# Performance work log

Hardware: AMD Instinct MI355X
Metric: run time of the kernel (lower is better)

## Reference

```python
import jax, jax.numpy as jnp
import numpy as np

N_EVENTS = 16384   # original pixel events
D = 128            # input_size
H = 128            # hidden_size
K = 9              # kernel 3x3 -> patch coords
S = 2048           # number of patch sequences
LMAX = 108         # max sequence length
T = 147456         # total patch events = sum(lengths) = 9 * N_EVENTS


def setup_inputs() -> dict:
    key = jax.random.key(0)
    ks = jax.random.split(key, 8)
    events = jax.random.normal(ks[0], (N_EVENTS, D), jnp.float32)
    pos_id = jax.random.randint(ks[1], (T,), 0, K, dtype=jnp.int32)
    orig_event_idx = jax.random.randint(ks[2], (T,), 0, N_EVENTS, dtype=jnp.int32)
    # alternating 36/108 lengths: 1024*36 + 1024*108 = 147456 = T
    lengths = jnp.where(jnp.arange(S) % 2 == 0, 36, 108).astype(jnp.int32)
    std = float(np.sqrt(2.0 / (D + H)))
    scatter_w = jax.random.normal(ks[3], (K, H, D), jnp.float32) * std
    gather_w = jax.random.normal(ks[4], (K, H, H), jnp.float32) * std
    lstm_std = float(1.0 / np.sqrt(H))
    w_ih = jax.random.uniform(ks[5], (4 * H, H), jnp.float32, -lstm_std, lstm_std)
    w_hh = jax.random.uniform(ks[6], (4 * H, H), jnp.float32, -lstm_std, lstm_std)
    ln_g = jnp.ones((H,), jnp.float32)
    ln_b = jnp.zeros((H,), jnp.float32)
    return dict(events=events, scatter_w=scatter_w, gather_w=gather_w,
                w_ih=w_ih, w_hh=w_hh, ln_g=ln_g, ln_b=ln_b,
                pos_id=pos_id, orig_event_idx=orig_event_idx, lengths=lengths)


def _pos_proj(x, W, pos_id):
    # position-indexed projection: out[t] = W[pos_id[t]] @ x[t]
    # loop over small fixed K=9 with masked accumulate (matches the torch loop)
    out = jnp.zeros((x.shape[0], W.shape[1]), x.dtype)
    for k in range(W.shape[0]):
        out = out + jnp.where((pos_id == k)[:, None], x @ W[k].T, 0.0)
    return out


def reference(events, scatter_w, gather_w, w_ih, w_hh, ln_g, ln_b,
              pos_id, orig_event_idx, lengths):
    # scatter events to patch replicas
    x = events[orig_event_idx]                           # [T, D]
    x = _pos_proj(x, scatter_w, pos_id)                  # [T, H]

    # flat (sequence-major) -> padded [S, LMAX, H]
    seq_offsets = jnp.cumsum(lengths) - lengths          # [S]
    seq_ids = jnp.repeat(jnp.arange(S), lengths, total_repeat_length=T)
    pos_in_seq = jnp.arange(T) - seq_offsets[seq_ids]
    padded = jnp.zeros((S, LMAX, H), x.dtype).at[seq_ids, pos_in_seq].set(x)

    # single-layer bias-free LSTM (pytorch gate order i, f, g, o), zero init.
    # zero-padding after each sequence's valid region leaves valid outputs
    # identical to a PackedSequence LSTM.
    def step(carry, xt):                                 # xt: [S, H]
        h, c = carry
        gates = xt @ w_ih.T + h @ w_hh.T                 # [S, 4H]
        i, f, g, o = jnp.split(gates, 4, axis=-1)
        c = jax.nn.sigmoid(f) * c + jax.nn.sigmoid(i) * jnp.tanh(g)
        h = jax.nn.sigmoid(o) * jnp.tanh(c)
        return (h, c), h

    init = (jnp.zeros((S, H), x.dtype), jnp.zeros((S, H), x.dtype))
    _, hs = jax.lax.scan(step, init, jnp.swapaxes(padded, 0, 1))  # [LMAX, S, H]
    o_flat = jnp.swapaxes(hs, 0, 1)[seq_ids, pos_in_seq]          # [T, H]

    o_flat = _pos_proj(o_flat, gather_w, pos_id)                  # [T, H]

    # gather patch events back to pixel events (scatter-add) + residual + LN
    out = jnp.zeros((N_EVENTS, H), x.dtype).at[orig_event_idx].add(o_flat)
    out = out + events                                   # input_proj is None (D == H)
    mu = jnp.mean(out, axis=-1, keepdims=True)
    var = jnp.var(out, axis=-1, keepdims=True)
    out = (out - mu) * jax.lax.rsqrt(var + 1e-5) * ln_g + ln_b
    return out
```

## Files before the change

kernel.cpp:

```cpp
#include <hip/hip_runtime.h>

#define N_EVENTS 16384
#define DIM 128
#define NK 9
#define NSEQ 2048
#define TT 147456
#define CHUNK 64
#define NCHUNK_MAX (TT/CHUNK + NK)
#define NHBLK 576

typedef __attribute__((ext_vector_type(8))) short bf16x8;
typedef __attribute__((ext_vector_type(4))) float f32x4;
typedef __attribute__((ext_vector_type(4))) int i32x4;

#define OFF_EV     0UL
#define OFF_WC     (OFF_EV   + (size_t)N_EVENTS*DIM*2)
#define OFF_SCAT   (OFF_WC   + (size_t)512*256*2)
#define OFF_GATH   (OFF_SCAT + (size_t)NK*DIM*DIM*2)
#define OFF_XS     (OFF_GATH + (size_t)NK*DIM*DIM*2)
#define OFF_HS     (OFF_XS   + (size_t)TT*DIM*2)
#define OFF_KLIST  (OFF_HS   + (size_t)TT*DIM*2)
#define OFF_ACC    (OFF_KLIST+ (size_t)TT*4)
#define OFF_SEQOFF (OFF_ACC  + (size_t)N_EVENTS*DIM*4)
#define OFF_GROUP  (OFF_SEQOFF + (size_t)NSEQ*4)
#define OFF_MISC   (OFF_GROUP  + (size_t)NSEQ*4)
#define OFF_BH     (OFF_MISC   + 256UL)

__device__ __forceinline__ short f2b(float f) {
    union { float f; unsigned u; } v; v.f = f;
    unsigned r = (v.u + 0x7FFFu + ((v.u >> 16) & 1u)) >> 16;
    return (short)r;
}

__device__ __forceinline__ float fsig(float x) {
    return __builtin_amdgcn_rcpf(1.f + __expf(-x));
}
__device__ __forceinline__ float ftanh(float x) {
    return 1.f - 2.f * __builtin_amdgcn_rcpf(__expf(2.f * x) + 1.f);
}

__global__ void convert_kernel(const float* __restrict__ ev, const float* __restrict__ wih,
                               const float* __restrict__ whh, const float* __restrict__ sw,
                               const float* __restrict__ gw,
                               short* __restrict__ evb, short* __restrict__ wcb,
                               short* __restrict__ swb, short* __restrict__ gwb,
                               float* __restrict__ acc) {
    int idx = blockIdx.x * blockDim.x + threadIdx.x;
    if (idx < N_EVENTS * DIM) { evb[idx] = f2b(ev[idx]); acc[idx] = 0.f; }
    if (idx < 512 * DIM) {
        int j = idx >> 7, d = idx & 127;
        wcb[j * 256 + d]       = f2b(wih[idx]);
        wcb[j * 256 + 128 + d] = f2b(whh[idx]);
    }
    if (idx < NK * DIM * DIM) { swb[idx] = f2b(sw[idx]); gwb[idx] = f2b(gw[idx]); }
}

__global__ void hist_kernel(const int* __restrict__ pos, int* __restrict__ blockhist) {
    __shared__ int h[NK];
    int tid = threadIdx.x;
    if (tid < NK) h[tid] = 0;
    __syncthreads();
    atomicAdd(&h[pos[blockIdx.x * 256 + tid]], 1);
    __syncthreads();
    if (tid < NK) blockhist[blockIdx.x * NK + tid] = h[tid];
}

__global__ void scan_kernel(int* __restrict__ blockhist, int* __restrict__ misc) {
    __shared__ int h[NHBLK * NK];
    int tid = threadIdx.x;
    for (int i = tid; i < NHBLK * NK; i += 256) h[i] = blockhist[i];
    __syncthreads();
    if (tid < NK) {
        int run = 0;
        for (int b = 0; b < NHBLK; b++) {
            int v = h[b * NK + tid];
            h[b * NK + tid] = run;
            run += v;
        }
        misc[tid] = run;
    }
    __syncthreads();
    if (tid == 0) {
        int ko = 0, co = 0;
        for (int k = 0; k < NK; k++) {
            int c = misc[k];
            misc[32 + k] = ko;
            misc[48 + k] = co;
            ko += c;
            co += (c + CHUNK - 1) / CHUNK;
        }
        misc[48 + NK] = co;
    }
    __syncthreads();
    for (int i = tid; i < NHBLK * NK; i += 256) blockhist[i] = h[i];
}

__global__ void setup_kernel(const int* __restrict__ lengths,
                             int* __restrict__ seq_off, int* __restrict__ grouped) {
    __shared__ int lens[NSEQ];
    __shared__ int tsum[256], tlong[256];
    int tid = threadIdx.x;
    for (int i = tid; i < NSEQ; i += 256) lens[i] = lengths[i];
    __syncthreads();
    int base = tid * 8;
    int ls[8]; int s = 0, lc = 0;
    #pragma unroll
    for (int i = 0; i < 8; i++) { ls[i] = lens[base + i]; s += ls[i]; lc += (ls[i] > 64) ? 1 : 0; }
    tsum[tid] = s; tlong[tid] = lc;
    __syncthreads();
    for (int d = 1; d < 256; d <<= 1) {
        int a = (tid >= d) ? tsum[tid - d] : 0;
        int b = (tid >= d) ? tlong[tid - d] : 0;
        __syncthreads();
        tsum[tid] += a; tlong[tid] += b;
        __syncthreads();
    }
    int nlong_total = tlong[255];
    int excl = tsum[tid] - s;
    int excl_long = tlong[tid] - lc;
    int run = 0, runl = 0;
    #pragma unroll
    for (int i = 0; i < 8; i++) {
        int sid = base + i;
        seq_off[sid] = excl + run;
        int longs_before = excl_long + runl;
        if (ls[i] > 64) { grouped[longs_before] = sid; runl++; }
        else            { grouped[nlong_total + (sid - longs_before)] = sid; }
        run += ls[i];
    }
}

__global__ void fill2_kernel(const int* __restrict__ pos, const int* __restrict__ blockhist,
                             const int* __restrict__ misc, int* __restrict__ klist) {
    __shared__ int off[NK];
    int tid = threadIdx.x;
    if (tid < NK) off[tid] = misc[32 + tid] + blockhist[blockIdx.x * NK + tid];
    __syncthreads();
    int t = blockIdx.x * 256 + tid;
    int p = atomicAdd(&off[pos[t]], 1);
    klist[p] = t;
}

__global__ void bucket_gemm(const short* __restrict__ src, const short* __restrict__ wall,
                            const int* __restrict__ klist, const int* __restrict__ misc,
                            const int* __restrict__ orig, short* __restrict__ xs_out,
                            float* __restrict__ acc, int mode) {
    const int* chunkoff = misc + 48;
    int b = blockIdx.x;
    if (b >= chunkoff[NK]) return;
    int k = 0;
    while (k < NK - 1 && chunkoff[k + 1] <= b) k++;
    int lc = b - chunkoff[k];
    int cnt = misc[k];
    int base = misc[32 + k] + lc * CHUNK;
    int nv = min(CHUNK, cnt - lc * CHUNK);

    __shared__ int tok[CHUNK], dst[CHUNK];
    __shared__ short A[CHUNK * 136];
    int tid = threadIdx.x;
    if (tid < CHUNK) {
        int tv = klist[base + ((tid < nv) ? tid : 0)];
        tok[tid] = tv;
        dst[tid] = orig[tv];
    }
    __syncthreads();
    {
        int row = tid >> 2, part = tid & 3;
        int ridx = (mode == 0) ? dst[row] : tok[row];
        const i32x4* s4 = (const i32x4*)(src + (size_t)ridx * DIM + part * 32);
        i32x4* d4 = (i32x4*)(A + row * 136 + part * 32);
        d4[0] = s4[0]; d4[1] = s4[1]; d4[2] = s4[2]; d4[3] = s4[3];
    }
    __syncthreads();
    int wave = tid >> 6, lane = tid & 63, l15 = lane & 15, q = lane >> 4;
    const short* wk = wall + (size_t)k * DIM * DIM;
    bf16x8 Bf[2][4];
    #pragma unroll
    for (int nt = 0; nt < 2; nt++) {
        int h = wave * 32 + nt * 16 + l15;
        #pragma unroll
        for (int kt = 0; kt < 4; kt++)
            Bf[nt][kt] = *(const bf16x8*)(wk + h * DIM + kt * 32 + q * 8);
    }
    f32x4 C[4][2];
    #pragma unroll
    for (int mt = 0; mt < 4; mt++)
        #pragma unroll
        for (int nt = 0; nt < 2; nt++) C[mt][nt] = (f32x4){0.f, 0.f, 0.f, 0.f};
    #pragma unroll
    for (int mt = 0; mt < 4; mt++) {
        bf16x8 Afr[4];
        const short* ar = A + (mt * 16 + l15) * 136 + q * 8;
        Afr[0] = *(const bf16x8*)(ar);
        Afr[1] = *(const bf16x8*)(ar + 32);
        Afr[2] = *(const bf16x8*)(ar + 64);
        Afr[3] = *(const bf16x8*)(ar + 96);
        #pragma unroll
        for (int nt = 0; nt < 2; nt++)
            #pragma unroll
            for (int kt = 0; kt < 4; kt++)
                C[mt][nt] = __builtin_amdgcn_mfma_f32_16x16x32_bf16(Afr[kt], Bf[nt][kt], C[mt][nt], 0, 0, 0);
    }
    if (mode == 0) {
        __syncthreads();
        #pragma unroll
        for (int mt = 0; mt < 4; mt++)
            #pragma unroll
            for (int nt = 0; nt < 2; nt++)
                #pragma unroll
                for (int r = 0; r < 4; r++) {
                    int row = mt * 16 + q * 4 + r;
                    int col = wave * 32 + nt * 16 + l15;
                    A[row * 136 + col] = f2b(C[mt][nt][r]);
                }
        __syncthreads();
        int row = tid >> 2, part = tid & 3;
        if (row < nv) {
            const i32x4* s4 = (const i32x4*)(A + row * 136 + part * 32);
            i32x4* d4 = (i32x4*)(xs_out + (size_t)tok[row] * DIM + part * 32);
            d4[0] = s4[0]; d4[1] = s4[1]; d4[2] = s4[2]; d4[3] = s4[3];
        }
    } else {
        #pragma unroll
        for (int mt = 0; mt < 4; mt++)
            #pragma unroll
            for (int nt = 0; nt < 2; nt++)
                #pragma unroll
                for (int r = 0; r < 4; r++) {
                    int row = mt * 16 + q * 4 + r;
                    if (row < nv) {
                        int col = wave * 32 + nt * 16 + l15;
                        atomicAdd(acc + (size_t)dst[row] * DIM + col, C[mt][nt][r]);
                    }
                }
    }
}

#define MF(a, b, c) __builtin_amdgcn_mfma_f32_16x16x32_bf16(a, b, c, 0, 0, 0)

#define LSTM_STEP(J, PF) { \
    const int i_ = ib8 + (J); \
    f32x4 Cxi = {0.f,0.f,0.f,0.f}, Cxf = {0.f,0.f,0.f,0.f}; \
    f32x4 Cxg = {0.f,0.f,0.f,0.f}, Cxo = {0.f,0.f,0.f,0.f}; \
    Cxi = MF(PF[0], Bf[0][0], Cxi); Cxf = MF(PF[0], Bf[1][0], Cxf); \
    Cxg = MF(PF[0], Bf[2][0], Cxg); Cxo = MF(PF[0], Bf[3][0], Cxo); \
    Cxi = MF(PF[1], Bf[0][1], Cxi); Cxf = MF(PF[1], Bf[1][1], Cxf); \
    Cxg = MF(PF[1], Bf[2][1], Cxg); Cxo = MF(PF[1], Bf[3][1], Cxo); \
    Cxi = MF(PF[2], Bf[0][2], Cxi); Cxf = MF(PF[2], Bf[1][2], Cxf); \
    Cxg = MF(PF[2], Bf[2][2], Cxg); Cxo = MF(PF[2], Bf[3][2], Cxo); \
    Cxi = MF(PF[3], Bf[0][3], Cxi); Cxf = MF(PF[3], Bf[1][3], Cxf); \
    Cxg = MF(PF[3], Bf[2][3], Cxg); Cxo = MF(PF[3], Bf[3][3], Cxo); \
    bf16x8 Hf0, Hf1, Hf2, Hf3; \
    { const short* hp_ = hb + (((J) + 7) & 7) * 1088 + l15 * 136 + ql * 8; \
      Hf0 = *(const bf16x8*)(hp_);      Hf1 = *(const bf16x8*)(hp_ + 32); \
      Hf2 = *(const bf16x8*)(hp_ + 64); Hf3 = *(const bf16x8*)(hp_ + 96); } \
    f32x4 Chi = {0.f,0.f,0.f,0.f}, Chf = {0.f,0.f,0.f,0.f}; \
    f32x4 Chg = {0.f,0.f,0.f,0.f}, Cho = {0.f,0.f,0.f,0.f}; \
    Chi = MF(Hf0, Bf[0][4], Chi); Chf = MF(Hf0, Bf[1][4], Chf); \
    Chg = MF(Hf0, Bf[2][4], Chg); Cho = MF(Hf0, Bf[3][4], Cho); \
    Chi = MF(Hf1, Bf[0][5], Chi); Chf = MF(Hf1, Bf[1][5], Chf); \
    Chg = MF(Hf1, Bf[2][5], Chg); Cho = MF(Hf1, Bf[3][5], Cho); \
    Chi = MF(Hf2, Bf[0][6], Chi); Chf = MF(Hf2, Bf[1][6], Chf); \
    Chg = MF(Hf2, Bf[2][6], Chg); Cho = MF(Hf2, Bf[3][6], Cho); \
    Chi = MF(Hf3, Bf[0][7], Chi); Chf = MF(Hf3, Bf[1][7], Chf); \
    Chg = MF(Hf3, Bf[2][7], Chg); Cho = MF(Hf3, Bf[3][7], Cho); \
    if (l15 < 8) { \
        const short* xp_ = xs + xoff; \
        PF[0] = *(const bf16x8*)(xp_);      PF[1] = *(const bf16x8*)(xp_ + 32); \
        PF[2] = *(const bf16x8*)(xp_ + 64); PF[3] = *(const bf16x8*)(xp_ + 96); \
    } \
    xoff += ((i_ + 4) <= my_len) ? DIM : 0; \
    f32x4 Gi = Cxi + Chi, Gf = Cxf + Chf, Gg = Cxg + Chg, Go = Cxo + Cho; \
    { \
        int src_ = lane & 31; \
        float i2 = __shfl(Gi[2], src_, 64), i3 = __shfl(Gi[3], src_, 64); \
        float f2 = __shfl(Gf[2], src_, 64), f3 = __shfl(Gf[3], src_, 64); \
        float g2 = __shfl(Gg[2], src_, 64), g3 = __shfl(Gg[3], src_, 64); \
        float o2 = __shfl(Go[2], src_, 64), o3 = __shfl(Go[3], src_, 64); \
        float iA = lo ? Gi[0] : i2, iB = lo ? Gi[1] : i3; \
        float fA = lo ? Gf[0] : f2, fB = lo ? Gf[1] : f3; \
        float gA = lo ? Gg[0] : g2, gB = lo ? Gg[1] : g3; \
        float oA = lo ? Go[0] : o2, oB = lo ? Go[1] : o3; \
        if (i_ < lenA) { \
            float si = fsig(iA), sf = fsig(fA), so = fsig(oA); \
            float tg = ftanh(gA); \
            float cn = sf * cA + si * tg; \
            float th = ftanh(cn); \
            cA = cn; \
            hb[(J) * 1088 + rowA * 136 + u] = f2b(so * th); \
        } \
        if (i_ < lenB) { \
            float si = fsig(iB), sf = fsig(fB), so = fsig(oB); \
            float tg = ftanh(gB); \
            float cn = sf * cB + si * tg; \
            float th = ftanh(cn); \
            cB = cn; \
            hb[(J) * 1088 + rowB * 136 + u] = f2b(so * th); \
        } \
    } \
    __syncthreads(); \
}

__global__ __launch_bounds__(512, 2) void lstm_kernel(
        const short* __restrict__ xs, const short* __restrict__ wc,
        short* __restrict__ hstore, const int* __restrict__ seq_off,
        const int* __restrict__ grouped, const int* __restrict__ lengths) {
    __shared__ int s_off[8], s_len[8];
    __shared__ short hchunk[11][8][136];
    int tid = threadIdx.x;
    if (tid < 8) {
        int s = grouped[blockIdx.x * 8 + tid];
        s_off[tid] = seq_off[s];
        s_len[tid] = lengths[s];
    }
    for (int j = tid; j < 11 * 8 * 136; j += 512) ((short*)hchunk)[j] = 0;
    __syncthreads();
    int lane = tid & 63, l15 = lane & 15, ql = lane >> 4;
    int wave = tid >> 6;
    int u = wave * 16 + l15;
    short* hb = (short*)hchunk;
    bf16x8 Bf[4][8];
    #pragma unroll
    for (int g = 0; g < 4; g++) {
        int j = g * 128 + u;
        #pragma unroll
        for (int kt = 0; kt < 8; kt++)
            Bf[g][kt] = *(const bf16x8*)(wc + j * 256 + kt * 32 + ql * 8);
    }
    int maxlen = 0;
    #pragma unroll
    for (int i = 0; i < 8; i++) maxlen = max(maxlen, s_len[i]);
    int my_off = (l15 < 8) ? s_off[l15] : 0;
    int my_len = (l15 < 8) ? s_len[l15] : 1;
    bool lo = (ql < 2);
    int rowA = lo ? (ql * 4 + 0) : ((ql - 2) * 4 + 2);
    int rowB = lo ? (ql * 4 + 1) : ((ql - 2) * 4 + 3);
    int lenA = s_len[rowA], lenB = s_len[rowB];
    float cA = 0.f, cB = 0.f;
    bf16x8 Pf0[4], Pf1[4];
    #pragma unroll
    for (int k = 0; k < 4; k++) { Pf0[k] = (bf16x8){0,0,0,0,0,0,0,0}; Pf1[k] = Pf0[k]; }
    int xoff = my_off * DIM + ql * 8;
    if (l15 < 8) {
        const short* xp = xs + xoff;
        Pf0[0] = *(const bf16x8*)(xp);      Pf0[1] = *(const bf16x8*)(xp + 32);
        Pf0[2] = *(const bf16x8*)(xp + 64); Pf0[3] = *(const bf16x8*)(xp + 96);
    }
    int xoff1 = xoff + ((my_len > 1) ? DIM : 0);
    if (l15 < 8) {
        const short* xp = xs + xoff1;
        Pf1[0] = *(const bf16x8*)(xp);      Pf1[1] = *(const bf16x8*)(xp + 32);
        Pf1[2] = *(const bf16x8*)(xp + 64); Pf1[3] = *(const bf16x8*)(xp + 96);
    }
    xoff = xoff1 + ((my_len > 2) ? DIM : 0);

    int nb8 = (maxlen + 7) >> 3;
    for (int ob = 0; ob < nb8; ob++) {
        int ib8 = ob * 8;
        LSTM_STEP(0, Pf0)
        LSTM_STEP(1, Pf1)
        LSTM_STEP(2, Pf0)
        LSTM_STEP(3, Pf1)
        LSTM_STEP(4, Pf0)
        LSTM_STEP(5, Pf1)
        LSTM_STEP(6, Pf0)
        LSTM_STEP(7, Pf1)
        #pragma unroll
        for (int it = 0; it < 2; it++) {
            int idx = tid + it * 512;
            int st = idx >> 7, s = (idx >> 4) & 7, part = idx & 15;
            int ig = ib8 + st;
            if (ig < s_len[s]) {
                i32x4 v = *(const i32x4*)&hchunk[st][s][part * 8];
                *(i32x4*)(hstore + (size_t)(s_off[s] + ig) * DIM + part * 8) = v;
            }
        }
        __syncthreads();
    }
}

__global__ void ln_kernel(const float* __restrict__ acc, const float* __restrict__ events,
                          const float* __restrict__ g, const float* __restrict__ bta,
                          float* __restrict__ out) {
    int tid = threadIdx.x;
    int wave = tid >> 6, lane = tid & 63;
    int e = blockIdx.x * 4 + wave;
    const float2* a2 = (const float2*)(acc + (size_t)e * DIM);
    const float2* e2 = (const float2*)(events + (size_t)e * DIM);
    float2 av = a2[lane], ev = e2[lane];
    float x0 = av.x + ev.x, x1 = av.y + ev.y;
    float sm = x0 + x1, sq = x0 * x0 + x1 * x1;
    #pragma unroll
    for (int m = 1; m < 64; m <<= 1) {
        sm += __shfl_xor(sm, m, 64);
        sq += __shfl_xor(sq, m, 64);
    }
    float mean = sm * (1.f / DIM);
    float var = sq * (1.f / DIM) - mean * mean;
    float rs = rsqrtf(var + 1e-5f);
    float2 gv = ((const float2*)g)[lane], bv = ((const float2*)bta)[lane];
    float2 ov;
    ov.x = (x0 - mean) * rs * gv.x + bv.x;
    ov.y = (x1 - mean) * rs * gv.y + bv.y;
    ((float2*)(out + (size_t)e * DIM))[lane] = ov;
}

extern "C" void kernel_launch(void* const* d_in, const int* in_sizes, int n_in,
                              void* d_out, int out_size, void* d_ws, size_t ws_size,
                              hipStream_t stream) {
    const float* events = (const float*)d_in[0];
    const float* scat   = (const float*)d_in[1];
    const float* gath   = (const float*)d_in[2];
    const float* wih    = (const float*)d_in[3];
    const float* whh    = (const float*)d_in[4];
    const float* lng    = (const float*)d_in[5];
    const float* lnb    = (const float*)d_in[6];
    const int* posid    = (const int*)d_in[7];
    const int* orig     = (const int*)d_in[8];
    const int* lens     = (const int*)d_in[9];
    char* ws = (char*)d_ws;
    short* evb   = (short*)(ws + OFF_EV);
    short* wcb   = (short*)(ws + OFF_WC);
    short* swb   = (short*)(ws + OFF_SCAT);
    short* gwb   = (short*)(ws + OFF_GATH);
    short* xs    = (short*)(ws + OFF_XS);
    short* hs    = (short*)(ws + OFF_HS);
    int*   klist = (int*)(ws + OFF_KLIST);
    float* acc   = (float*)(ws + OFF_ACC);
    int*   seqo  = (int*)(ws + OFF_SEQOFF);
    int*   grp   = (int*)(ws + OFF_GROUP);
    int*   misc  = (int*)(ws + OFF_MISC);
    int*   bh    = (int*)(ws + OFF_BH);
    float* out   = (float*)d_out;

    convert_kernel<<<8192, 256, 0, stream>>>(events, wih, whh, scat, gath, evb, wcb, swb, gwb, acc);
    hist_kernel<<<NHBLK, 256, 0, stream>>>(posid, bh);
    scan_kernel<<<1, 256, 0, stream>>>(bh, misc);
    setup_kernel<<<1, 256, 0, stream>>>(lens, seqo, grp);
    fill2_kernel<<<NHBLK, 256, 0, stream>>>(posid, bh, misc, klist);
    bucket_gemm<<<NCHUNK_MAX, 256, 0, stream>>>(evb, swb, klist, misc, orig, xs, nullptr, 0);
    lstm_kernel<<<256, 512, 0, stream>>>(xs, wcb, hs, seqo, grp, lens);
    bucket_gemm<<<NCHUNK_MAX, 256, 0, stream>>>(hs, gwb, klist, misc, orig, nullptr, acc, 1);
    ln_kernel<<<4096, 256, 0, stream>>>(acc, events, lng, lnb, out);
}
```

Before: 317.7 us.

## Fuse all pipeline stages into one cooperative persistent kernel with grid syncs

New measurement: 506.9 us. 1.6x slower.

```diff
diff --git a/kernel.cpp b/kernel.cpp
--- a/kernel.cpp
+++ b/kernel.cpp
@@ -1,4 +1,7 @@
 #include <hip/hip_runtime.h>
+#include <hip/hip_cooperative_groups.h>
+
+namespace cg = cooperative_groups;
 
 #define N_EVENTS 16384
 #define DIM 128
@@ -6,8 +9,9 @@
 #define NSEQ 2048
 #define TT 147456
 #define CHUNK 64
-#define NCHUNK_MAX (TT/CHUNK + NK)
-#define NHBLK 576
+#define NBLK 256
+#define TPB 512
+#define TOKB 576
 
 typedef __attribute__((ext_vector_type(8))) short bf16x8;
 typedef __attribute__((ext_vector_type(4))) float f32x4;
@@ -26,12 +30,19 @@
 #define OFF_MISC   (OFF_GROUP  + (size_t)NSEQ*4)
 #define OFF_BH     (OFF_MISC   + 256UL)
 
+struct MegaParams {
+    const float *ev, *sw, *gw, *wih, *whh, *lng, *lnb;
+    const int *pos, *orig, *lens;
+    short *evb, *wcb, *swb, *gwb, *xs, *hs;
+    int *klist, *misc, *bh, *seqo, *grp;
+    float *acc, *out;
+};
+
 __device__ __forceinline__ short f2b(float f) {
     union { float f; unsigned u; } v; v.f = f;
     unsigned r = (v.u + 0x7FFFu + ((v.u >> 16) & 1u)) >> 16;
     return (short)r;
 }
-
 __device__ __forceinline__ float fsig(float x) {
     return __builtin_amdgcn_rcpf(1.f + __expf(-x));
 }
@@ -39,125 +50,20 @@
     return 1.f - 2.f * __builtin_amdgcn_rcpf(__expf(2.f * x) + 1.f);
 }
 
-__global__ void convert_kernel(const float* __restrict__ ev, const float* __restrict__ wih,
-                               const float* __restrict__ whh, const float* __restrict__ sw,
-                               const float* __restrict__ gw,
-                               short* __restrict__ evb, short* __restrict__ wcb,
-                               short* __restrict__ swb, short* __restrict__ gwb,
-                               float* __restrict__ acc) {
-    int idx = blockIdx.x * blockDim.x + threadIdx.x;
-    if (idx < N_EVENTS * DIM) { evb[idx] = f2b(ev[idx]); acc[idx] = 0.f; }
-    if (idx < 512 * DIM) {
-        int j = idx >> 7, d = idx & 127;
-        wcb[j * 256 + d]       = f2b(wih[idx]);
-        wcb[j * 256 + 128 + d] = f2b(whh[idx]);
-    }
-    if (idx < NK * DIM * DIM) { swb[idx] = f2b(sw[idx]); gwb[idx] = f2b(gw[idx]); }
-}
-
-__global__ void hist_kernel(const int* __restrict__ pos, int* __restrict__ blockhist) {
-    __shared__ int h[NK];
-    int tid = threadIdx.x;
-    if (tid < NK) h[tid] = 0;
-    __syncthreads();
-    atomicAdd(&h[pos[blockIdx.x * 256 + tid]], 1);
-    __syncthreads();
-    if (tid < NK) blockhist[blockIdx.x * NK + tid] = h[tid];
-}
-
-__global__ void scan_kernel(int* __restrict__ blockhist, int* __restrict__ misc) {
-    __shared__ int h[NHBLK * NK];
-    int tid = threadIdx.x;
-    for (int i = tid; i < NHBLK * NK; i += 256) h[i] = blockhist[i];
-    __syncthreads();
-    if (tid < NK) {
-        int run = 0;
-        for (int b = 0; b < NHBLK; b++) {
-            int v = h[b * NK + tid];
-            h[b * NK + tid] = run;
-            run += v;
-        }
-        misc[tid] = run;
-    }
-    __syncthreads();
-    if (tid == 0) {
-        int ko = 0, co = 0;
-        for (int k = 0; k < NK; k++) {
-            int c = misc[k];
-            misc[32 + k] = ko;
-            misc[48 + k] = co;
-            ko += c;
-            co += (c + CHUNK - 1) / CHUNK;
-        }
-        misc[48 + NK] = co;
-    }
-    __syncthreads();
-    for (int i = tid; i < NHBLK * NK; i += 256) blockhist[i] = h[i];
-}
-
-__global__ void setup_kernel(const int* __restrict__ lengths,
-                             int* __restrict__ seq_off, int* __restrict__ grouped) {
-    __shared__ int lens[NSEQ];
-    __shared__ int tsum[256], tlong[256];
-    int tid = threadIdx.x;
-    for (int i = tid; i < NSEQ; i += 256) lens[i] = lengths[i];
-    __syncthreads();
-    int base = tid * 8;
-    int ls[8]; int s = 0, lc = 0;
+#define MF(a, b, c) __builtin_amdgcn_mfma_f32_16x16x32_bf16(a, b, c, 0, 0, 0)
+
+__device__ __forceinline__ void bucket_chunk(
+        int c, const int* choff, const short* src, const short* wall,
+        const int* klist, const int* misc, const int* orig,
+        short* xs_out, float* acc, int mode,
+        int* tok, int* dst, short* A, int tid) {
+    int k = 0;
     #pragma unroll
-    for (int i = 0; i < 8; i++) { ls[i] = lens[base + i]; s += ls[i]; lc += (ls[i] > 64) ? 1 : 0; }
-    tsum[tid] = s; tlong[tid] = lc;
-    __syncthreads();
-    for (int d = 1; d < 256; d <<= 1) {
-        int a = (tid >= d) ? tsum[tid - d] : 0;
-        int b = (tid >= d) ? tlong[tid - d] : 0;
-        __syncthreads();
-        tsum[tid] += a; tlong[tid] += b;
-        __syncthreads();
-    }
-    int nlong_total = tlong[255];
-    int excl = tsum[tid] - s;
-    int excl_long = tlong[tid] - lc;
-    int run = 0, runl = 0;
-    #pragma unroll
-    for (int i = 0; i < 8; i++) {
-        int sid = base + i;
-        seq_off[sid] = excl + run;
-        int longs_before = excl_long + runl;
-        if (ls[i] > 64) { grouped[longs_before] = sid; runl++; }
-        else            { grouped[nlong_total + (sid - longs_before)] = sid; }
-        run += ls[i];
-    }
-}
-
-__global__ void fill2_kernel(const int* __restrict__ pos, const int* __restrict__ blockhist,
-                             const int* __restrict__ misc, int* __restrict__ klist) {
-    __shared__ int off[NK];
-    int tid = threadIdx.x;
-    if (tid < NK) off[tid] = misc[32 + tid] + blockhist[blockIdx.x * NK + tid];
-    __syncthreads();
-    int t = blockIdx.x * 256 + tid;
-    int p = atomicAdd(&off[pos[t]], 1);
-    klist[p] = t;
-}
-
-__global__ void bucket_gemm(const short* __restrict__ src, const short* __restrict__ wall,
-                            const int* __restrict__ klist, const int* __restrict__ misc,
-                            const int* __restrict__ orig, short* __restrict__ xs_out,
-                            float* __restrict__ acc, int mode) {
-    const int* chunkoff = misc + 48;
-    int b = blockIdx.x;
-    if (b >= chunkoff[NK]) return;
-    int k = 0;
-    while (k < NK - 1 && chunkoff[k + 1] <= b) k++;
-    int lc = b - chunkoff[k];
+    for (int j = 1; j < NK; j++) k += (choff[j] <= c) ? 1 : 0;
+    int lc = c - choff[k];
     int cnt = misc[k];
     int base = misc[32 + k] + lc * CHUNK;
     int nv = min(CHUNK, cnt - lc * CHUNK);
-
-    __shared__ int tok[CHUNK], dst[CHUNK];
-    __shared__ short A[CHUNK * 136];
-    int tid = threadIdx.x;
     if (tid < CHUNK) {
         int tv = klist[base + ((tid < nv) ? tid : 0)];
         tok[tid] = tv;
@@ -165,78 +71,62 @@
     }
     __syncthreads();
     {
-        int row = tid >> 2, part = tid & 3;
+        int row = tid >> 3, part = tid & 7;
         int ridx = (mode == 0) ? dst[row] : tok[row];
-        const i32x4* s4 = (const i32x4*)(src + (size_t)ridx * DIM + part * 32);
-        i32x4* d4 = (i32x4*)(A + row * 136 + part * 32);
-        d4[0] = s4[0]; d4[1] = s4[1]; d4[2] = s4[2]; d4[3] = s4[3];
+        const i32x4* s4 = (const i32x4*)(src + (size_t)ridx * DIM + part * 16);
+        i32x4* d4 = (i32x4*)(A + row * 136 + part * 16);
+        d4[0] = s4[0]; d4[1] = s4[1];
     }
     __syncthreads();
-    int wave = tid >> 6, lane = tid & 63, l15 = lane & 15, q = lane >> 4;
+    int w = tid >> 6, lane = tid & 63, l15 = lane & 15, q = lane >> 4;
     const short* wk = wall + (size_t)k * DIM * DIM;
-    bf16x8 Bf[2][4];
+    int h = w * 16 + l15;
+    bf16x8 Bfr[4];
     #pragma unroll
-    for (int nt = 0; nt < 2; nt++) {
-        int h = wave * 32 + nt * 16 + l15;
-        #pragma unroll
-        for (int kt = 0; kt < 4; kt++)
-            Bf[nt][kt] = *(const bf16x8*)(wk + h * DIM + kt * 32 + q * 8);
-    }
-    f32x4 C[4][2];
+    for (int kt = 0; kt < 4; kt++)
+        Bfr[kt] = *(const bf16x8*)(wk + h * DIM + kt * 32 + q * 8);
+    f32x4 C[4];
     #pragma unroll
-    for (int mt = 0; mt < 4; mt++)
-        #pragma unroll
-        for (int nt = 0; nt < 2; nt++) C[mt][nt] = (f32x4){0.f, 0.f, 0.f, 0.f};
+    for (int mt = 0; mt < 4; mt++) C[mt] = (f32x4){0.f, 0.f, 0.f, 0.f};
     #pragma unroll
     for (int mt = 0; mt < 4; mt++) {
-        bf16x8 Afr[4];
         const short* ar = A + (mt * 16 + l15) * 136 + q * 8;
-        Afr[0] = *(const bf16x8*)(ar);
-        Afr[1] = *(const bf16x8*)(ar + 32);
-        Afr[2] = *(const bf16x8*)(ar + 64);
-        Afr[3] = *(const bf16x8*)(ar + 96);
-        #pragma unroll
-        for (int nt = 0; nt < 2; nt++)
-            #pragma unroll
-            for (int kt = 0; kt < 4; kt++)
-                C[mt][nt] = __builtin_amdgcn_mfma_f32_16x16x32_bf16(Afr[kt], Bf[nt][kt], C[mt][nt], 0, 0, 0);
+        bf16x8 A0 = *(const bf16x8*)(ar);
+        bf16x8 A1 = *(const bf16x8*)(ar + 32);
+        bf16x8 A2 = *(const bf16x8*)(ar + 64);
+        bf16x8 A3 = *(const bf16x8*)(ar + 96);
+        C[mt] = MF(A0, Bfr[0], C[mt]);
+        C[mt] = MF(A1, Bfr[1], C[mt]);
+        C[mt] = MF(A2, Bfr[2], C[mt]);
+        C[mt] = MF(A3, Bfr[3], C[mt]);
     }
     if (mode == 0) {
         __syncthreads();
         #pragma unroll
         for (int mt = 0; mt < 4; mt++)
             #pragma unroll
-            for (int nt = 0; nt < 2; nt++)
-                #pragma unroll
-                for (int r = 0; r < 4; r++) {
-                    int row = mt * 16 + q * 4 + r;
-                    int col = wave * 32 + nt * 16 + l15;
-                    A[row * 136 + col] = f2b(C[mt][nt][r]);
-                }
-        __syncthreads();
-        int row = tid >> 2, part = tid & 3;
+            for (int r = 0; r < 4; r++)
+                A[(mt * 16 + q * 4 + r) * 136 + h] = f2b(C[mt][r]);
+        __syncthreads();
+        int row = tid >> 3, part = tid & 7;
         if (row < nv) {
-            const i32x4* s4 = (const i32x4*)(A + row * 136 + part * 32);
-            i32x4* d4 = (i32x4*)(xs_out + (size_t)tok[row] * DIM + part * 32);
-            d4[0] = s4[0]; d4[1] = s4[1]; d4[2] = s4[2]; d4[3] = s4[3];
-        }
+            const i32x4* s4 = (const i32x4*)(A + row * 136 + part * 16);
+            i32x4* d4 = (i32x4*)(xs_out + (size_t)tok[row] * DIM + part * 16);
+            d4[0] = s4[0]; d4[1] = s4[1];
+        }
+        __syncthreads();
     } else {
         #pragma unroll
         for (int mt = 0; mt < 4; mt++)
             #pragma unroll
-            for (int nt = 0; nt < 2; nt++)
-                #pragma unroll
-                for (int r = 0; r < 4; r++) {
-                    int row = mt * 16 + q * 4 + r;
-                    if (row < nv) {
-                        int col = wave * 32 + nt * 16 + l15;
-                        atomicAdd(acc + (size_t)dst[row] * DIM + col, C[mt][nt][r]);
-                    }
-                }
-    }
-}
-
-#define MF(a, b, c) __builtin_amdgcn_mfma_f32_16x16x32_bf16(a, b, c, 0, 0, 0)
+            for (int r = 0; r < 4; r++) {
+                int row = mt * 16 + q * 4 + r;
+                if (row < nv)
+                    atomicAdd(acc + (size_t)dst[row] * DIM + h, C[mt][r]);
+            }
+        __syncthreads();
+    }
+}
 
 #define LSTM_STEP(J, PF) { \
     const int i_ = ib8 + (J); \
@@ -265,7 +155,7 @@
     Chi = MF(Hf3, Bf[0][7], Chi); Chf = MF(Hf3, Bf[1][7], Chf); \
     Chg = MF(Hf3, Bf[2][7], Chg); Cho = MF(Hf3, Bf[3][7], Cho); \
     if (l15 < 8) { \
-        const short* xp_ = xs + xoff; \
+        const short* xp_ = xsl + xoff; \
         PF[0] = *(const bf16x8*)(xp_);      PF[1] = *(const bf16x8*)(xp_ + 32); \
         PF[2] = *(const bf16x8*)(xp_ + 64); PF[3] = *(const bf16x8*)(xp_ + 96); \
     } \
@@ -301,145 +191,281 @@
     __syncthreads(); \
 }
 
-__global__ __launch_bounds__(512, 2) void lstm_kernel(
-        const short* __restrict__ xs, const short* __restrict__ wc,
-        short* __restrict__ hstore, const int* __restrict__ seq_off,
-        const int* __restrict__ grouped, const int* __restrict__ lengths) {
+__global__ __launch_bounds__(TPB, 2) void mega_kernel(MegaParams p) {
+    cg::grid_group grid = cg::this_grid();
+    __shared__ int hist9[NK];
+    __shared__ int hsc[NBLK * NK];
+    __shared__ int cnt9[NK];
+    __shared__ int lensS[NSEQ];
+    __shared__ int tsum[256], tlong[256];
+    __shared__ int offb[NK];
+    __shared__ int tok[CHUNK], dst[CHUNK];
+    __shared__ short Atile[CHUNK * 136];
+    __shared__ short hchunk[11 * 8 * 136];
     __shared__ int s_off[8], s_len[8];
-    __shared__ short hchunk[11][8][136];
-    int tid = threadIdx.x;
-    if (tid < 8) {
-        int s = grouped[blockIdx.x * 8 + tid];
-        s_off[tid] = seq_off[s];
-        s_len[tid] = lengths[s];
-    }
-    for (int j = tid; j < 11 * 8 * 136; j += 512) ((short*)hchunk)[j] = 0;
+
+    const int bid = blockIdx.x, tid = threadIdx.x;
+    const int gtid = bid * TPB + tid;
+
+    for (int i = gtid; i < N_EVENTS * DIM; i += NBLK * TPB) {
+        p.evb[i] = f2b(p.ev[i]);
+        p.acc[i] = 0.f;
+    }
+    if (gtid < 512 * DIM) {
+        int j = gtid >> 7, d = gtid & 127;
+        p.wcb[j * 256 + d]       = f2b(p.wih[gtid]);
+        p.wcb[j * 256 + 128 + d] = f2b(p.whh[gtid]);
+    }
+    for (int i = gtid; i < NK * DIM * DIM; i += NBLK * TPB) {
+        p.swb[i] = f2b(p.sw[i]);
+        p.gwb[i] = f2b(p.gw[i]);
+    }
+    if (tid < NK) hist9[tid] = 0;
     __syncthreads();
-    int lane = tid & 63, l15 = lane & 15, ql = lane >> 4;
-    int wave = tid >> 6;
-    int u = wave * 16 + l15;
-    short* hb = (short*)hchunk;
-    bf16x8 Bf[4][8];
-    #pragma unroll
-    for (int g = 0; g < 4; g++) {
-        int j = g * 128 + u;
-        #pragma unroll
-        for (int kt = 0; kt < 8; kt++)
-            Bf[g][kt] = *(const bf16x8*)(wc + j * 256 + kt * 32 + ql * 8);
-    }
-    int maxlen = 0;
-    #pragma unroll
-    for (int i = 0; i < 8; i++) maxlen = max(maxlen, s_len[i]);
-    int my_off = (l15 < 8) ? s_off[l15] : 0;
-    int my_len = (l15 < 8) ? s_len[l15] : 1;
-    bool lo = (ql < 2);
-    int rowA = lo ? (ql * 4 + 0) : ((ql - 2) * 4 + 2);
-    int rowB = lo ? (ql * 4 + 1) : ((ql - 2) * 4 + 3);
-    int lenA = s_len[rowA], lenB = s_len[rowB];
-    float cA = 0.f, cB = 0.f;
-    bf16x8 Pf0[4], Pf1[4];
-    #pragma unroll
-    for (int k = 0; k < 4; k++) { Pf0[k] = (bf16x8){0,0,0,0,0,0,0,0}; Pf1[k] = Pf0[k]; }
-    int xoff = my_off * DIM + ql * 8;
-    if (l15 < 8) {
-        const short* xp = xs + xoff;
-        Pf0[0] = *(const bf16x8*)(xp);      Pf0[1] = *(const bf16x8*)(xp + 32);
-        Pf0[2] = *(const bf16x8*)(xp + 64); Pf0[3] = *(const bf16x8*)(xp + 96);
-    }
-    int xoff1 = xoff + ((my_len > 1) ? DIM : 0);
-    if (l15 < 8) {
-        const short* xp = xs + xoff1;
-        Pf1[0] = *(const bf16x8*)(xp);      Pf1[1] = *(const bf16x8*)(xp + 32);
-        Pf1[2] = *(const bf16x8*)(xp + 64); Pf1[3] = *(const bf16x8*)(xp + 96);
-    }
-    xoff = xoff1 + ((my_len > 2) ? DIM : 0);
-
-    int nb8 = (maxlen + 7) >> 3;
-    for (int ob = 0; ob < nb8; ob++) {
-        int ib8 = ob * 8;
-        LSTM_STEP(0, Pf0)
-        LSTM_STEP(1, Pf1)
-        LSTM_STEP(2, Pf0)
-        LSTM_STEP(3, Pf1)
-        LSTM_STEP(4, Pf0)
-        LSTM_STEP(5, Pf1)
-        LSTM_STEP(6, Pf0)
-        LSTM_STEP(7, Pf1)
-        #pragma unroll
-        for (int it = 0; it < 2; it++) {
-            int idx = tid + it * 512;
-            int st = idx >> 7, s = (idx >> 4) & 7, part = idx & 15;
-            int ig = ib8 + st;
-            if (ig < s_len[s]) {
-                i32x4 v = *(const i32x4*)&hchunk[st][s][part * 8];
-                *(i32x4*)(hstore + (size_t)(s_off[s] + ig) * DIM + part * 8) = v;
-            }
-        }
-        __syncthreads();
-    }
-}
-
-__global__ void ln_kernel(const float* __restrict__ acc, const float* __restrict__ events,
-                          const float* __restrict__ g, const float* __restrict__ bta,
-                          float* __restrict__ out) {
-    int tid = threadIdx.x;
-    int wave = tid >> 6, lane = tid & 63;
-    int e = blockIdx.x * 4 + wave;
-    const float2* a2 = (const float2*)(acc + (size_t)e * DIM);
-    const float2* e2 = (const float2*)(events + (size_t)e * DIM);
-    float2 av = a2[lane], ev = e2[lane];
-    float x0 = av.x + ev.x, x1 = av.y + ev.y;
-    float sm = x0 + x1, sq = x0 * x0 + x1 * x1;
-    #pragma unroll
-    for (int m = 1; m < 64; m <<= 1) {
-        sm += __shfl_xor(sm, m, 64);
-        sq += __shfl_xor(sq, m, 64);
-    }
-    float mean = sm * (1.f / DIM);
-    float var = sq * (1.f / DIM) - mean * mean;
-    float rs = rsqrtf(var + 1e-5f);
-    float2 gv = ((const float2*)g)[lane], bv = ((const float2*)bta)[lane];
-    float2 ov;
-    ov.x = (x0 - mean) * rs * gv.x + bv.x;
-    ov.y = (x1 - mean) * rs * gv.y + bv.y;
-    ((float2*)(out + (size_t)e * DIM))[lane] = ov;
+    {
+        int t0 = bid * TOKB + tid;
+        atomicAdd(&hist9[p.pos[t0]], 1);
+        if (tid < TOKB - TPB) atomicAdd(&hist9[p.pos[t0 + TPB]], 1);
+    }
+    __syncthreads();
+    if (tid < NK) p.bh[bid * NK + tid] = hist9[tid];
+    grid.sync();
+
+    if (bid == 0) {
+        for (int i = tid; i < NBLK * NK; i += TPB) hsc[i] = p.bh[i];
+        __syncthreads();
+        if (tid < NK) {
+            int run = 0;
+            for (int b = 0; b < NBLK; b++) {
+                int v = hsc[b * NK + tid];
+                hsc[b * NK + tid] = run;
+                run += v;
+            }
+            cnt9[tid] = run;
+            p.misc[tid] = run;
+        }
+        __syncthreads();
+        if (tid == 0) {
+            int ko = 0, co = 0;
+            for (int k = 0; k < NK; k++) {
+                int c = cnt9[k];
+                p.misc[32 + k] = ko;
+                p.misc[48 + k] = co;
+                ko += c;
+                co += (c + CHUNK - 1) / CHUNK;
+            }
+            p.misc[48 + NK] = co;
+        }
+        for (int i = tid; i < NBLK * NK; i += TPB) p.bh[i] = hsc[i];
+    }
+    if (bid == 1) {
+        for (int i = tid; i < NSEQ; i += TPB) lensS[i] = p.lens[i];
+        __syncthreads();
+        int base = tid * 8;
+        int ls[8]; int s = 0, lc = 0;
+        if (tid < 256) {
+            #pragma unroll
+            for (int i = 0; i < 8; i++) {
+                ls[i] = lensS[base + i]; s += ls[i]; lc += (ls[i] > 64) ? 1 : 0;
+            }
+            tsum[tid] = s; tlong[tid] = lc;
+        }
+        __syncthreads();
+        for (int d = 1; d < 256; d <<= 1) {
+            int a = 0, b = 0;
+            if (tid < 256 && tid >= d) { a = tsum[tid - d]; b = tlong[tid - d]; }
+            __syncthreads();
+            if (tid < 256) { tsum[tid] += a; tlong[tid] += b; }
+            __syncthreads();
+        }
+        if (tid < 256) {
+            int nlong_total = tlong[255];
+            int excl = tsum[tid] - s;
+            int excl_long = tlong[tid] - lc;
+            int run = 0, runl = 0;
+            #pragma unroll
+            for (int i = 0; i < 8; i++) {
+                int sid = base + i;
+                p.seqo[sid] = excl + run;
+                int lb = excl_long + runl;
+                if (ls[i] > 64) { p.grp[lb] = sid; runl++; }
+                else            { p.grp[nlong_total + (sid - lb)] = sid; }
+                run += ls[i];
+            }
+        }
+    }
+    grid.sync();
+
+    if (tid < NK) offb[tid] = p.misc[32 + tid] + p.bh[bid * NK + tid];
+    __syncthreads();
+    {
+        int t0 = bid * TOKB + tid;
+        int pos0 = p.pos[t0];
+        int r0 = atomicAdd(&offb[pos0], 1);
+        p.klist[r0] = t0;
+        if (tid < TOKB - TPB) {
+            int t1 = t0 + TPB;
+            int pos1 = p.pos[t1];
+            int r1 = atomicAdd(&offb[pos1], 1);
+            p.klist[r1] = t1;
+        }
+    }
+    grid.sync();
+
+    {
+        int choff[NK + 1];
+        #pragma unroll
+        for (int j = 0; j <= NK; j++) choff[j] = p.misc[48 + j];
+        int nchunks = choff[NK];
+        for (int c = bid; c < nchunks; c += NBLK)
+            bucket_chunk(c, choff, p.evb, p.swb, p.klist, p.misc, p.orig,
+                         p.xs, nullptr, 0, tok, dst, Atile, tid);
+    }
+    grid.sync();
+
+    {
+        const short* xsl = p.xs;
+        const short* wc = p.wcb;
+        short* hstore = p.hs;
+        if (tid < 8) {
+            int s = p.grp[bid * 8 + tid];
+            s_off[tid] = p.seqo[s];
+            s_len[tid] = p.lens[s];
+        }
+        for (int j = tid; j < 11 * 8 * 136; j += TPB) hchunk[j] = 0;
+        __syncthreads();
+        int lane = tid & 63, l15 = lane & 15, ql = lane >> 4;
+        int wave = tid >> 6;
+        int u = wave * 16 + l15;
+        short* hb = hchunk;
+        bf16x8 Bf[4][8];
+        #pragma unroll
+        for (int g = 0; g < 4; g++) {
+            int j = g * 128 + u;
+            #pragma unroll
+            for (int kt = 0; kt < 8; kt++)
+                Bf[g][kt] = *(const bf16x8*)(wc + j * 256 + kt * 32 + ql * 8);
+        }
+        int maxlen = 0;
+        #pragma unroll
+        for (int i = 0; i < 8; i++) maxlen = max(maxlen, s_len[i]);
+        int my_off = (l15 < 8) ? s_off[l15] : 0;
+        int my_len = (l15 < 8) ? s_len[l15] : 1;
+        bool lo = (ql < 2);
+        int rowA = lo ? (ql * 4 + 0) : ((ql - 2) * 4 + 2);
+        int rowB = lo ? (ql * 4 + 1) : ((ql - 2) * 4 + 3);
+        int lenA = s_len[rowA], lenB = s_len[rowB];
+        float cA = 0.f, cB = 0.f;
+        bf16x8 Pf0[4], Pf1[4];
+        #pragma unroll
+        for (int k = 0; k < 4; k++) { Pf0[k] = (bf16x8){0,0,0,0,0,0,0,0}; Pf1[k] = Pf0[k]; }
+        int xoff = my_off * DIM + ql * 8;
+        if (l15 < 8) {
+            const short* xp = xsl + xoff;
+            Pf0[0] = *(const bf16x8*)(xp);      Pf0[1] = *(const bf16x8*)(xp + 32);
+            Pf0[2] = *(const bf16x8*)(xp + 64); Pf0[3] = *(const bf16x8*)(xp + 96);
+        }
+        int xoff1 = xoff + ((my_len > 1) ? DIM : 0);
+        if (l15 < 8) {
+            const short* xp = xsl + xoff1;
+            Pf1[0] = *(const bf16x8*)(xp);      Pf1[1] = *(const bf16x8*)(xp + 32);
+            Pf1[2] = *(const bf16x8*)(xp + 64); Pf1[3] = *(const bf16x8*)(xp + 96);
+        }
+        xoff = xoff1 + ((my_len > 2) ? DIM : 0);
+
+        int nb8 = (maxlen + 7) >> 3;
+        for (int ob = 0; ob < nb8; ob++) {
+            int ib8 = ob * 8;
+            LSTM_STEP(0, Pf0)
+            LSTM_STEP(1, Pf1)
+            LSTM_STEP(2, Pf0)
+            LSTM_STEP(3, Pf1)
+            LSTM_STEP(4, Pf0)
+            LSTM_STEP(5, Pf1)
+            LSTM_STEP(6, Pf0)
+            LSTM_STEP(7, Pf1)
+            #pragma unroll
+            for (int it = 0; it < 2; it++) {
+                int idx = tid + it * TPB;
+                int st = idx >> 7, s = (idx >> 4) & 7, part = idx & 15;
+                int ig = ib8 + st;
+                if (ig < s_len[s]) {
+                    i32x4 v = *(const i32x4*)&hchunk[st * 1088 + s * 136 + part * 8];
+                    *(i32x4*)(hstore + (size_t)(s_off[s] + ig) * DIM + part * 8) = v;
+                }
+            }
+            __syncthreads();
+        }
+    }
+    grid.sync();
+
+    {
+        int choff[NK + 1];
+        #pragma unroll
+        for (int j = 0; j <= NK; j++) choff[j] = p.misc[48 + j];
+        int nchunks = choff[NK];
+        for (int c = bid; c < nchunks; c += NBLK)
+            bucket_chunk(c, choff, p.hs, p.gwb, p.klist, p.misc, p.orig,
+                         nullptr, p.acc, 1, tok, dst, Atile, tid);
+    }
+    grid.sync();
+
+    {
+        int wave = tid >> 6, lane = tid & 63;
+        for (int pass = 0; pass < 8; pass++) {
+            int e = bid * 8 + wave + pass * 2048;
+            const float2* a2 = (const float2*)(p.acc + (size_t)e * DIM);
+            const float2* e2 = (const float2*)(p.ev + (size_t)e * DIM);
+            float2 av = a2[lane], ev = e2[lane];
+            float x0 = av.x + ev.x, x1 = av.y + ev.y;
+            float sm = x0 + x1, sq = x0 * x0 + x1 * x1;
+            #pragma unroll
+            for (int m = 1; m < 64; m <<= 1) {
+                sm += __shfl_xor(sm, m, 64);
+                sq += __shfl_xor(sq, m, 64);
+            }
+            float mean = sm * (1.f / DIM);
+            float var = sq * (1.f / DIM) - mean * mean;
+            float rs = rsqrtf(var + 1e-5f);
+            float2 gv = ((const float2*)p.lng)[lane], bv = ((const float2*)p.lnb)[lane];
+            float2 ov;
+            ov.x = (x0 - mean) * rs * gv.x + bv.x;
+            ov.y = (x1 - mean) * rs * gv.y + bv.y;
+            ((float2*)(p.out + (size_t)e * DIM))[lane] = ov;
+        }
+    }
 }
 
 extern "C" void kernel_launch(void* const* d_in, const int* in_sizes, int n_in,
                               void* d_out, int out_size, void* d_ws, size_t ws_size,
                               hipStream_t stream) {
-    const float* events = (const float*)d_in[0];
-    const float* scat   = (const float*)d_in[1];
-    const float* gath   = (const float*)d_in[2];
-    const float* wih    = (const float*)d_in[3];
-    const float* whh    = (const float*)d_in[4];
-    const float* lng    = (const float*)d_in[5];
-    const float* lnb    = (const float*)d_in[6];
-    const int* posid    = (const int*)d_in[7];
-    const int* orig     = (const int*)d_in[8];
-    const int* lens     = (const int*)d_in[9];
     char* ws = (char*)d_ws;
-    short* evb   = (short*)(ws + OFF_EV);
-    short* wcb   = (short*)(ws + OFF_WC);
-    short* swb   = (short*)(ws + OFF_SCAT);
-    short* gwb   = (short*)(ws + OFF_GATH);
-    short* xs    = (short*)(ws + OFF_XS);
-    short* hs    = (short*)(ws + OFF_HS);
-    int*   klist = (int*)(ws + OFF_KLIST);
-    float* acc   = (float*)(ws + OFF_ACC);
-    int*   seqo  = (int*)(ws + OFF_SEQOFF);
-    int*   grp   = (int*)(ws + OFF_GROUP);
-    int*   misc  = (int*)(ws + OFF_MISC);
-    int*   bh    = (int*)(ws + OFF_BH);
-    float* out   = (float*)d_out;
-
-    convert_kernel<<<8192, 256, 0, stream>>>(events, wih, whh, scat, gath, evb, wcb, swb, gwb, acc);
-    hist_kernel<<<NHBLK, 256, 0, stream>>>(posid, bh);
-    scan_kernel<<<1, 256, 0, stream>>>(bh, misc);
-    setup_kernel<<<1, 256, 0, stream>>>(lens, seqo, grp);
-    fill2_kernel<<<NHBLK, 256, 0, stream>>>(posid, bh, misc, klist);
-    bucket_gemm<<<NCHUNK_MAX, 256, 0, stream>>>(evb, swb, klist, misc, orig, xs, nullptr, 0);
-    lstm_kernel<<<256, 512, 0, stream>>>(xs, wcb, hs, seqo, grp, lens);
-    bucket_gemm<<<NCHUNK_MAX, 256, 0, stream>>>(hs, gwb, klist, misc, orig, nullptr, acc, 1);
-    ln_kernel<<<4096, 256, 0, stream>>>(acc, events, lng, lnb, out);
-}
+    MegaParams p;
+    p.ev    = (const float*)d_in[0];
+    p.sw    = (const float*)d_in[1];
+    p.gw    = (const float*)d_in[2];
+    p.wih   = (const float*)d_in[3];
+    p.whh   = (const float*)d_in[4];
+    p.lng   = (const float*)d_in[5];
+    p.lnb   = (const float*)d_in[6];
+    p.pos   = (const int*)d_in[7];
+    p.orig  = (const int*)d_in[8];
+    p.lens  = (const int*)d_in[9];
+    p.evb   = (short*)(ws + OFF_EV);
+    p.wcb   = (short*)(ws + OFF_WC);
+    p.swb   = (short*)(ws + OFF_SCAT);
+    p.gwb   = (short*)(ws + OFF_GATH);
+    p.xs    = (short*)(ws + OFF_XS);
+    p.hs    = (short*)(ws + OFF_HS);
+    p.klist = (int*)(ws + OFF_KLIST);
+    p.acc   = (float*)(ws + OFF_ACC);
+    p.seqo  = (int*)(ws + OFF_SEQOFF);
+    p.grp   = (int*)(ws + OFF_GROUP);
+    p.misc  = (int*)(ws + OFF_MISC);
+    p.bh    = (int*)(ws + OFF_BH);
+    p.out   = (float*)d_out;
+
+    void* kargs[] = { (void*)&p };
+    hipLaunchCooperativeKernel((const void*)mega_kernel, dim3(NBLK), dim3(TPB),
+                               kargs, 0, stream);
+}
```
